# Kernel tuning notes

Hardware: AMD Instinct MI355X
Metric: run time of the kernel (lower is better)

The kernel has to match this reference:

```python
import jax, jax.numpy as jnp
import numpy as np

N_NODES = 100000
N_EDGES = 1000000
D_FEAT = 64
N_FILTER = 64
N_CLASSES = 16


def gcn_norm(edge_idx, n):
    """Add self-loops and compute symmetric normalization D^-1/2 (A+I) D^-1/2."""
    loop = jnp.arange(n, dtype=edge_idx.dtype)
    src = jnp.concatenate([edge_idx[0], loop])  # [E+N]
    dst = jnp.concatenate([edge_idx[1], loop])  # [E+N]
    w = jnp.ones(src.shape[0], dtype=jnp.float32)
    deg = jax.ops.segment_sum(w, dst, num_segments=n)  # in-degree incl. self-loop
    dinv = jnp.where(deg > 0, jax.lax.rsqrt(deg), 0.0)
    norm = dinv[src] * w * dinv[dst]  # [E+N]
    return src, dst, norm


def gcn_conv(x, W, b, src, dst, norm, n):
    h = x @ W                                   # [n, f] dense transform first (f <= d)
    msg = h[src] * norm[:, None]                # gather + scale  [E+N, f]
    out = jax.ops.segment_sum(msg, dst, num_segments=n)  # scatter-add  [n, f]
    return out + b


def setup_inputs() -> dict:
    key = jax.random.key(0)
    k1, k2, k3, k4 = jax.random.split(key, 4)
    X = jax.random.normal(k1, (N_NODES, D_FEAT), dtype=jnp.float32)
    edge_idx = jax.random.randint(k2, (2, N_EDGES), 0, N_NODES, dtype=jnp.int64)
    W1 = jax.random.normal(k3, (D_FEAT, N_FILTER), dtype=jnp.float32) * 0.05
    b1 = jnp.zeros((N_FILTER,), dtype=jnp.float32)
    W2 = jax.random.normal(k4, (N_FILTER, N_CLASSES), dtype=jnp.float32) * 0.05
    b2 = jnp.zeros((N_CLASSES,), dtype=jnp.float32)
    return {"X": X, "edge_idx": edge_idx, "W1": W1, "b1": b1, "W2": W2, "b2": b2}


def reference(X, edge_idx, W1, b1, W2, b2):
    n = X.shape[0]
    src, dst, norm = gcn_norm(edge_idx, n)
    x = gcn_conv(X, W1, b1, src, dst, norm, n)
    x = jax.nn.relu(x)
    # dropout p=0 -> identity
    x = gcn_conv(x, W2, b2, src, dst, norm, n)
    return x  # raw logits; pred_layer is not applied in the torch forward
```

## Files before the change

### kernel.cpp

```cpp
#include <hip/hip_runtime.h>
#include <hip/hip_bf16.h>


constexpr int N = 100000;
constexpr int E = 1000000;
constexpr int NB = (N + 511) / 512;
constexpr int CAP = 6144;
constexpr int CSTRIDE = 32;
constexpr int CHUNK = 2048;
constexpr int NBLK = (E + CHUNK - 1) / CHUNK;
constexpr int BT = 512;
constexpr int NPW = 6;
constexpr int NW = (N + NPW - 1) / NPW;
constexpr int NWBLK = (NW + 3) / 4;

__device__ __forceinline__ float bflo(unsigned u) { return __uint_as_float(u << 16); }
__device__ __forceinline__ float bfhi(unsigned u) { return __uint_as_float(u & 0xffff0000u); }

__device__ __forceinline__ void wait_lgkm0() {
    __builtin_amdgcn_s_waitcnt(0xc07f);
    __builtin_amdgcn_sched_barrier(0);
}

__global__ void k_bfill(const int* __restrict__ src, const int* __restrict__ dst,
                        int* __restrict__ cursor, int* __restrict__ bkt) {
    __shared__ int hist[256];
    __shared__ int lbase[256];
    __shared__ int gbase[256];
    __shared__ int lcur[256];
    __shared__ int ws[8];
    __shared__ int stage[CHUNK];
    __shared__ unsigned char sbkt[CHUNK];
    int t = threadIdx.x;
    int lane = t & 63;
    int e0 = blockIdx.x * CHUNK;
    int cnt = min(CHUNK, E - e0);

    if (t < 256) hist[t] = 0;
    __syncthreads();
    for (int j = t; j < cnt; j += BT)
        atomicAdd(&hist[dst[e0 + j] >> 9], 1);
    __syncthreads();
    int h = (t < 256) ? hist[t] : 0;
    int v = h;
#pragma unroll
    for (int off = 1; off < 64; off <<= 1) {
        int u = __shfl_up(v, off);
        if (lane >= off) v += u;
    }
    if (lane == 63) ws[t >> 6] = v;
    __syncthreads();
    int add = 0;
    for (int i = 0; i < (t >> 6); ++i) add += ws[i];
    int inc = v + add;
    if (t < 256) { lbase[t] = inc - h; lcur[t] = 0; }
    if (t < NB) gbase[t] = h ? atomicAdd(&cursor[t * CSTRIDE], h) : 0;
    __syncthreads();
    for (int j = t; j < cnt; j += BT) {
        int d = dst[e0 + j];
        int b = d >> 9;
        int pos = lbase[b] + atomicAdd(&lcur[b], 1);
        stage[pos] = ((d & 511) << 17) | src[e0 + j];
        sbkt[pos] = (unsigned char)b;
    }
    __syncthreads();
    for (int j = t; j < cnt; j += BT) {
        int b = sbkt[j];
        int gpos = gbase[b] + (j - lbase[b]);
        if (gpos < CAP) bkt[b * CAP + gpos] = stage[j];
    }
}

__global__ void k_bfine(const int* __restrict__ cursor, const int* __restrict__ bkt,
                        int* __restrict__ row_ptr, float* __restrict__ dinv,
                        int* __restrict__ csr_src) {
    __shared__ int cnt[512];
    __shared__ int excl[512];
    __shared__ int ws[8];
    int b = blockIdx.x;
    int t = threadIdx.x;
    int lane = t & 63;
    int c = (t < NB) ? cursor[t * CSTRIDE] : 0;
    int mv = (t < b) ? c : 0;
#pragma unroll
    for (int off = 1; off < 64; off <<= 1) mv += __shfl_xor(mv, off);
    if (lane == 0) ws[t >> 6] = mv;
    cnt[t] = 0;
    __syncthreads();
    int base = ws[0] + ws[1] + ws[2] + ws[3] + ws[4] + ws[5] + ws[6] + ws[7];
    int m = cursor[b * CSTRIDE];
    if (b == 0 && t == 0) row_ptr[N] = E;
    const int* bb = bkt + b * CAP;
    const int4* bb4 = (const int4*)bb;
    int m4 = m >> 2;
    for (int j = t; j < m4; j += BT) {
        int4 v = bb4[j];
        atomicAdd(&cnt[v.x >> 17], 1); atomicAdd(&cnt[v.y >> 17], 1);
        atomicAdd(&cnt[v.z >> 17], 1); atomicAdd(&cnt[v.w >> 17], 1);
    }
    for (int j = (m4 << 2) + t; j < m; j += BT) atomicAdd(&cnt[bb[j] >> 17], 1);
    __syncthreads();
    int h = cnt[t];
    int v = h;
#pragma unroll
    for (int off = 1; off < 64; off <<= 1) {
        int u = __shfl_up(v, off);
        if (lane >= off) v += u;
    }
    if (lane == 63) ws[t >> 6] = v;
    __syncthreads();
    int add = 0;
    for (int i = 0; i < (t >> 6); ++i) add += ws[i];
    int ex = v + add - h;
    excl[t] = ex;
    int node = b * 512 + t;
    if (node < N) {
        row_ptr[node] = base + ex;
        dinv[node] = rsqrtf((float)(h + 1));
    }
    __syncthreads();
    for (int j = t; j < m4; j += BT) {
        int4 v4 = bb4[j];
        int p0 = atomicAdd(&excl[v4.x >> 17], 1); csr_src[base + p0] = v4.x & 0x1FFFF;
        int p1 = atomicAdd(&excl[v4.y >> 17], 1); csr_src[base + p1] = v4.y & 0x1FFFF;
        int p2 = atomicAdd(&excl[v4.z >> 17], 1); csr_src[base + p2] = v4.z & 0x1FFFF;
        int p3 = atomicAdd(&excl[v4.w >> 17], 1); csr_src[base + p3] = v4.w & 0x1FFFF;
    }
    for (int j = (m4 << 2) + t; j < m; j += BT) {
        int vv = bb[j];
        int p = atomicAdd(&excl[vv >> 17], 1);
        csr_src[base + p] = vv & 0x1FFFF;
    }
}

__global__ void k_gemm1(const float* __restrict__ X, const float* __restrict__ W1,
                        const float* __restrict__ dinv, __hip_bfloat16* __restrict__ h1s,
                        __hip_bfloat16* __restrict__ h2s) {
    __shared__ float sX[4][4][64];
    int t = threadIdx.x;
    int lane = t & 63;
    int w = t >> 6;
    int wid = (blockIdx.x * 256 + t) >> 6;
    if (blockIdx.x == 0) {
        if (t < 64) h1s[(size_t)N * 64 + t] = __float2bfloat16(0.f);
        if (t < 16) h2s[(size_t)N * 16 + t] = __float2bfloat16(0.f);
    }
    float w1[64];
#pragma unroll
    for (int k = 0; k < 64; ++k) w1[k] = W1[k * 64 + lane];
    constexpr int STRIDE = 4096 * 4;
    int r4 = wid * 4;
    float x0 = X[(size_t)r4 * 64 + lane];
    float x1 = X[(size_t)(r4 + 1) * 64 + lane];
    float x2 = X[(size_t)(r4 + 2) * 64 + lane];
    float x3 = X[(size_t)(r4 + 3) * 64 + lane];
    for (; r4 < N; r4 += STRIDE) {
        int rn = r4 + STRIDE;
        float y0 = 0.f, y1 = 0.f, y2 = 0.f, y3 = 0.f;
        if (rn < N) {
            y0 = X[(size_t)rn * 64 + lane];
            y1 = X[(size_t)(rn + 1) * 64 + lane];
            y2 = X[(size_t)(rn + 2) * 64 + lane];
            y3 = X[(size_t)(rn + 3) * 64 + lane];
        }
        float dv0 = dinv[r4], dv1 = dinv[r4 + 1], dv2 = dinv[r4 + 2], dv3 = dinv[r4 + 3];
        sX[w][0][lane] = x0; sX[w][1][lane] = x1;
        sX[w][2][lane] = x2; sX[w][3][lane] = x3;
        wait_lgkm0();
        float acc0 = 0.f, acc1 = 0.f, acc2 = 0.f, acc3 = 0.f;
#pragma unroll
        for (int k = 0; k < 64; ++k) {
            float wk = w1[k];
            acc0 = fmaf(sX[w][0][k], wk, acc0);
            acc1 = fmaf(sX[w][1][k], wk, acc1);
            acc2 = fmaf(sX[w][2][k], wk, acc2);
            acc3 = fmaf(sX[w][3][k], wk, acc3);
        }
        acc0 *= dv0; acc1 *= dv1; acc2 *= dv2; acc3 *= dv3;
        float up0 = __shfl_xor(acc0, 1);
        float up1 = __shfl_xor(acc1, 1);
        float up2 = __shfl_xor(acc2, 1);
        float up3 = __shfl_xor(acc3, 1);
        if (!(lane & 1)) {
            __hip_bfloat162 p;
            p.x = __float2bfloat16(acc0); p.y = __float2bfloat16(up0);
            *(__hip_bfloat162*)(h1s + (size_t)r4 * 64 + lane) = p;
            p.x = __float2bfloat16(acc1); p.y = __float2bfloat16(up1);
            *(__hip_bfloat162*)(h1s + (size_t)(r4 + 1) * 64 + lane) = p;
            p.x = __float2bfloat16(acc2); p.y = __float2bfloat16(up2);
            *(__hip_bfloat162*)(h1s + (size_t)(r4 + 2) * 64 + lane) = p;
            p.x = __float2bfloat16(acc3); p.y = __float2bfloat16(up3);
            *(__hip_bfloat162*)(h1s + (size_t)(r4 + 3) * 64 + lane) = p;
        }
        x0 = y0; x1 = y1; x2 = y2; x3 = y3;
    }
}

__global__ void k_layer12(const int* __restrict__ row_ptr, const int* __restrict__ csr_src,
                          const float* __restrict__ dinv, const __hip_bfloat16* __restrict__ h1s,
                          const float* __restrict__ b1, const float* __restrict__ W2,
                          __hip_bfloat16* __restrict__ h2s) {
    __shared__ float sy[4][8][72];
    int t = threadIdx.x;
    int lane = t & 63;
    int w = t >> 6;
    int g8 = lane >> 3;
    int qo = (lane & 7) << 4;
    int g16 = lane >> 4, c16 = lane & 15;
    int wid = blockIdx.x * 4 + w;
    int d0 = wid * NPW;
    if (d0 >= N) return;
    int dend = min(d0 + NPW, N);
    float w2[16];
#pragma unroll
    for (int j = 0; j < 16; ++j) w2[j] = W2[(g16 * 16 + j) * 16 + c16];
    float b1v = b1[lane];
    const char* Hb = (const char*)h1s;

    int rp0 = row_ptr[d0];
    for (int d = d0; d < dend; ++d) {
        int rp1 = row_ptr[d + 1];
        float dv = dinv[d];
        float a[8] = {0, 0, 0, 0, 0, 0, 0, 0};
        if (g8 == 0) {
            uint4 u = *(const uint4*)(Hb + (((unsigned)d << 7) | qo));
            a[0] = bflo(u.x); a[1] = bfhi(u.x); a[2] = bflo(u.y); a[3] = bfhi(u.y);
            a[4] = bflo(u.z); a[5] = bfhi(u.z); a[6] = bflo(u.w); a[7] = bfhi(u.w);
        }
        for (int base = rp0; base < rp1; base += 64) {
            int nloc = min(64, rp1 - base);
            int sidx = (lane < nloc) ? csr_src[base + lane] : N;
            int steps = (nloc + 15) >> 4;
            for (int j = 0; j < steps; ++j) {
                int b0 = (j << 4) | g8;
                int s0 = __shfl(sidx, b0);
                int s1 = __shfl(sidx, b0 | 8);
                uint4 u0 = *(const uint4*)(Hb + (((unsigned)s0 << 7) | qo));
                uint4 u1 = *(const uint4*)(Hb + (((unsigned)s1 << 7) | qo));
                a[0] += bflo(u0.x); a[1] += bfhi(u0.x); a[2] += bflo(u0.y); a[3] += bfhi(u0.y);
                a[4] += bflo(u0.z); a[5] += bfhi(u0.z); a[6] += bflo(u0.w); a[7] += bfhi(u0.w);
                a[0] += bflo(u1.x); a[1] += bfhi(u1.x); a[2] += bflo(u1.y); a[3] += bfhi(u1.y);
                a[4] += bflo(u1.z); a[5] += bfhi(u1.z); a[6] += bflo(u1.w); a[7] += bfhi(u1.w);
            }
        }
        rp0 = rp1;
        float* row = &sy[w][g8][(lane & 7) << 3];
        *(float4*)row = make_float4(a[0], a[1], a[2], a[3]);
        *(float4*)(row + 4) = make_float4(a[4], a[5], a[6], a[7]);
        wait_lgkm0();
        float ysum = sy[w][0][lane] + sy[w][1][lane] + sy[w][2][lane] + sy[w][3][lane]
                   + sy[w][4][lane] + sy[w][5][lane] + sy[w][6][lane] + sy[w][7][lane];
        float y = fmaxf(fmaf(dv, ysum, b1v), 0.f);
        float o = 0.f;
#pragma unroll
        for (int j = 0; j < 16; ++j) o = fmaf(__shfl(y, (lane & 48) | j), w2[j], o);
        o += __shfl_xor(o, 16);
        o += __shfl_xor(o, 32);
        o *= dv;
        float oup = __shfl_xor(o, 1);
        if (lane < 16 && !(lane & 1)) {
            __hip_bfloat162 p;
            p.x = __float2bfloat16(o);
            p.y = __float2bfloat16(oup);
            *(__hip_bfloat162*)(h2s + (size_t)d * 16 + lane) = p;
        }
    }
}

__global__ void k_gather2(const int* __restrict__ row_ptr, const int* __restrict__ csr_src,
                          const float* __restrict__ dinv, const __hip_bfloat16* __restrict__ h2s,
                          const float* __restrict__ b2, float* __restrict__ out) {
    int t = threadIdx.x;
    int lane = t & 63;
    int g4 = lane >> 2;
    int q2 = lane & 3;
    int qo = q2 << 3;
    int wid = blockIdx.x * 4 + (t >> 6);
    int d0 = wid * NPW;
    if (d0 >= N) return;
    int dend = min(d0 + NPW, N);
    float b2v[4];
#pragma unroll
    for (int k = 0; k < 4; ++k) b2v[k] = b2[q2 * 4 + k];
    const char* Hb = (const char*)h2s;

    int rp0 = row_ptr[d0];
    for (int d = d0; d < dend; ++d) {
        int rp1 = row_ptr[d + 1];
        float dv = dinv[d];
        float a[4] = {0, 0, 0, 0};
        if (g4 == 0) {
            uint2 u = *(const uint2*)(Hb + (((unsigned)d << 5) | qo));
            a[0] = bflo(u.x); a[1] = bfhi(u.x); a[2] = bflo(u.y); a[3] = bfhi(u.y);
        }
        for (int base = rp0; base < rp1; base += 64) {
            int nloc = min(64, rp1 - base);
            int sidx = (lane < nloc) ? csr_src[base + lane] : N;
            int steps = (nloc + 15) >> 4;
            for (int j = 0; j < steps; ++j) {
                int s = __shfl(sidx, (j << 4) | g4);
                uint2 u = *(const uint2*)(Hb + (((unsigned)s << 5) | qo));
                a[0] += bflo(u.x); a[1] += bfhi(u.x);
                a[2] += bflo(u.y); a[3] += bfhi(u.y);
            }
        }
        rp0 = rp1;
#pragma unroll
        for (int k = 0; k < 4; ++k) {
            a[k] += __shfl_xor(a[k], 4);
            a[k] += __shfl_xor(a[k], 8);
            a[k] += __shfl_xor(a[k], 16);
            a[k] += __shfl_xor(a[k], 32);
        }
        if (lane < 4) {
            float4 r;
            r.x = fmaf(dv, a[0], b2v[0]);
            r.y = fmaf(dv, a[1], b2v[1]);
            r.z = fmaf(dv, a[2], b2v[2]);
            r.w = fmaf(dv, a[3], b2v[3]);
            *(float4*)(out + (size_t)d * 16 + q2 * 4) = r;
        }
    }
}

extern "C" void kernel_launch(void* const* d_in, const int* in_sizes, int n_in,
                              void* d_out, int out_size, void* d_ws, size_t ws_size,
                              hipStream_t stream) {
    const float* X  = (const float*)d_in[0];
    const int*   ei = (const int*)d_in[1];
    const float* W1 = (const float*)d_in[2];
    const float* b1 = (const float*)d_in[3];
    const float* W2 = (const float*)d_in[4];
    const float* b2 = (const float*)d_in[5];
    float* out = (float*)d_out;

    int* cursor  = (int*)d_ws;
    int* row_ptr = cursor + NB * CSTRIDE;
    int* bkt     = row_ptr + N + 4;
    int* csr_src = bkt + NB * CAP;
    float* dinv  = (float*)(csr_src + E);
    __hip_bfloat16* h1s = (__hip_bfloat16*)(dinv + N);
    __hip_bfloat16* h2s = h1s + (size_t)(N + 1) * 64;

    const int* src = ei;
    const int* dst = ei + E;

    hipMemsetAsync(cursor, 0, NB * CSTRIDE * sizeof(int), stream);
    k_bfill<<<NBLK, BT, 0, stream>>>(src, dst, cursor, bkt);
    k_bfine<<<NB, BT, 0, stream>>>(cursor, bkt, row_ptr, dinv, csr_src);
    k_gemm1<<<1024, 256, 0, stream>>>(X, W1, dinv, h1s, h2s);
    k_layer12<<<NWBLK, 256, 0, stream>>>(row_ptr, csr_src, dinv, h1s, b1, W2, h2s);
    k_gather2<<<NWBLK, 256, 0, stream>>>(row_ptr, csr_src, dinv, h2s, b2, out);
}
```

Before: 186.8 us.

## Batch per-warp edge index loads and prefetch next node's gathers in GCN layers

Both gather kernels now load row_ptr and dinv for all of a warp's nodes in one lane-parallel read. When the warp's total edge count fits in two 64-lane registers, they also load the whole csr_src range up front. The fast path software-pipelines the gathers: the first neighbour rows and self row for node k+1 are issued before node k's reduction and epilogue, hiding gather latency behind the serialized dependency chain. Warps with many edges fall back to the original loop. The cost is extra register pressure and more shuffles per neighbour select.

```diff
diff --git a/kernel.cpp b/kernel.cpp
--- a/kernel.cpp
+++ b/kernel.cpp
@@ -196,6 +196,11 @@
     }
 }
 
+__device__ __forceinline__ void acc8(float a[8], uint4 u) {
+    a[0] += bflo(u.x); a[1] += bfhi(u.x); a[2] += bflo(u.y); a[3] += bfhi(u.y);
+    a[4] += bflo(u.z); a[5] += bfhi(u.z); a[6] += bflo(u.w); a[7] += bfhi(u.w);
+}
+
 __global__ void k_layer12(const int* __restrict__ row_ptr, const int* __restrict__ csr_src,
                           const float* __restrict__ dinv, const __hip_bfloat16* __restrict__ h1s,
                           const float* __restrict__ b1, const float* __restrict__ W2,
@@ -210,17 +215,92 @@
     int wid = blockIdx.x * 4 + w;
     int d0 = wid * NPW;
     if (d0 >= N) return;
-    int dend = min(d0 + NPW, N);
+    int nd = min(NPW, N - d0);
     float w2[16];
 #pragma unroll
     for (int j = 0; j < 16; ++j) w2[j] = W2[(g16 * 16 + j) * 16 + c16];
     float b1v = b1[lane];
     const char* Hb = (const char*)h1s;
 
-    int rp0 = row_ptr[d0];
-    for (int d = d0; d < dend; ++d) {
-        int rp1 = row_ptr[d + 1];
-        float dv = dinv[d];
+    int rp_l = row_ptr[d0 + min(lane, nd)];
+    float dv_l = dinv[min(d0 + lane, N - 1)];
+    int rp_start = __shfl(rp_l, 0);
+    int nE = __shfl(rp_l, nd) - rp_start;
+
+    if (nE <= 112) {
+        int sidx0 = (lane < nE) ? csr_src[rp_start + lane] : N;
+        int sidx1 = (64 + lane < nE) ? csr_src[rp_start + 64 + lane] : N;
+        bool wide = nE > 64;
+        auto wsel = [&](int pos, int oend) -> int {
+            int s = __shfl(sidx0, pos & 63);
+            if (wide) {
+                int s1 = __shfl(sidx1, pos & 63);
+                if (pos >= 64) s = s1;
+            }
+            return (pos < oend) ? s : N;
+        };
+        int o0 = 0;
+        int o1 = __shfl(rp_l, 1) - rp_start;
+        int sA0 = wsel(o0 + g8, o1);
+        int sA1 = wsel(o0 + g8 + 8, o1);
+        uint4 uA0 = *(const uint4*)(Hb + (((unsigned)sA0 << 7) | qo));
+        uint4 uA1 = *(const uint4*)(Hb + (((unsigned)sA1 << 7) | qo));
+        uint4 uSA = {};
+        if (g8 == 0) uSA = *(const uint4*)(Hb + (((unsigned)d0 << 7) | qo));
+        for (int k = 0; k < nd; ++k) {
+            int d = d0 + k;
+            float dv = __shfl(dv_l, k);
+            int o0n = 0, o1n = 0;
+            uint4 uB0 = {}, uB1 = {}, uSB = {};
+            bool more = (k + 1 < nd);
+            if (more) {
+                o0n = __shfl(rp_l, k + 1) - rp_start;
+                o1n = __shfl(rp_l, k + 2) - rp_start;
+                int sB0 = wsel(o0n + g8, o1n);
+                int sB1 = wsel(o0n + g8 + 8, o1n);
+                uB0 = *(const uint4*)(Hb + (((unsigned)sB0 << 7) | qo));
+                uB1 = *(const uint4*)(Hb + (((unsigned)sB1 << 7) | qo));
+                if (g8 == 0) uSB = *(const uint4*)(Hb + (((unsigned)(d + 1) << 7) | qo));
+            }
+            float a[8] = {0, 0, 0, 0, 0, 0, 0, 0};
+            acc8(a, uA0); acc8(a, uA1);
+            if (g8 == 0) acc8(a, uSA);
+            for (int p = o0 + 16; p < o1; p += 16) {
+                int s0 = wsel(p + g8, o1);
+                int s1 = wsel(p + g8 + 8, o1);
+                uint4 u0 = *(const uint4*)(Hb + (((unsigned)s0 << 7) | qo));
+                uint4 u1 = *(const uint4*)(Hb + (((unsigned)s1 << 7) | qo));
+                acc8(a, u0); acc8(a, u1);
+            }
+            float* row = &sy[w][g8][(lane & 7) << 3];
+            *(float4*)row = make_float4(a[0], a[1], a[2], a[3]);
+            *(float4*)(row + 4) = make_float4(a[4], a[5], a[6], a[7]);
+            wait_lgkm0();
+            float ysum = sy[w][0][lane] + sy[w][1][lane] + sy[w][2][lane] + sy[w][3][lane]
+                       + sy[w][4][lane] + sy[w][5][lane] + sy[w][6][lane] + sy[w][7][lane];
+            float y = fmaxf(fmaf(dv, ysum, b1v), 0.f);
+            float o = 0.f;
+#pragma unroll
+            for (int j = 0; j < 16; ++j) o = fmaf(__shfl(y, (lane & 48) | j), w2[j], o);
+            o += __shfl_xor(o, 16);
+            o += __shfl_xor(o, 32);
+            o *= dv;
+            float oup = __shfl_xor(o, 1);
+            if (lane < 16 && !(lane & 1)) {
+                __hip_bfloat162 p;
+                p.x = __float2bfloat16(o);
+                p.y = __float2bfloat16(oup);
+                *(__hip_bfloat162*)(h2s + (size_t)d * 16 + lane) = p;
+            }
+            uA0 = uB0; uA1 = uB1; uSA = uSB; o0 = o0n; o1 = o1n;
+        }
+        return;
+    }
+    for (int k = 0; k < nd; ++k) {
+        int d = d0 + k;
+        int rp0 = __shfl(rp_l, k);
+        int rp1 = __shfl(rp_l, k + 1);
+        float dv = __shfl(dv_l, k);
         float a[8] = {0, 0, 0, 0, 0, 0, 0, 0};
         if (g8 == 0) {
             uint4 u = *(const uint4*)(Hb + (((unsigned)d << 7) | qo));
@@ -237,13 +317,9 @@
                 int s1 = __shfl(sidx, b0 | 8);
                 uint4 u0 = *(const uint4*)(Hb + (((unsigned)s0 << 7) | qo));
                 uint4 u1 = *(const uint4*)(Hb + (((unsigned)s1 << 7) | qo));
-                a[0] += bflo(u0.x); a[1] += bfhi(u0.x); a[2] += bflo(u0.y); a[3] += bfhi(u0.y);
-                a[4] += bflo(u0.z); a[5] += bfhi(u0.z); a[6] += bflo(u0.w); a[7] += bfhi(u0.w);
-                a[0] += bflo(u1.x); a[1] += bfhi(u1.x); a[2] += bflo(u1.y); a[3] += bfhi(u1.y);
-                a[4] += bflo(u1.z); a[5] += bfhi(u1.z); a[6] += bflo(u1.w); a[7] += bfhi(u1.w);
-            }
-        }
-        rp0 = rp1;
+                acc8(a, u0); acc8(a, u1);
+            }
+        }
         float* row = &sy[w][g8][(lane & 7) << 3];
         *(float4*)row = make_float4(a[0], a[1], a[2], a[3]);
         *(float4*)(row + 4) = make_float4(a[4], a[5], a[6], a[7]);
@@ -265,6 +341,10 @@
             *(__hip_bfloat162*)(h2s + (size_t)d * 16 + lane) = p;
         }
     }
+}
+
+__device__ __forceinline__ void acc4(float a[4], uint2 u) {
+    a[0] += bflo(u.x); a[1] += bfhi(u.x); a[2] += bflo(u.y); a[3] += bfhi(u.y);
 }
 
 __global__ void k_gather2(const int* __restrict__ row_ptr, const int* __restrict__ csr_src,
@@ -278,16 +358,80 @@
     int wid = blockIdx.x * 4 + (t >> 6);
     int d0 = wid * NPW;
     if (d0 >= N) return;
-    int dend = min(d0 + NPW, N);
+    int nd = min(NPW, N - d0);
     float b2v[4];
 #pragma unroll
     for (int k = 0; k < 4; ++k) b2v[k] = b2[q2 * 4 + k];
     const char* Hb = (const char*)h2s;
 
-    int rp0 = row_ptr[d0];
-    for (int d = d0; d < dend; ++d) {
-        int rp1 = row_ptr[d + 1];
-        float dv = dinv[d];
+    int rp_l = row_ptr[d0 + min(lane, nd)];
+    float dv_l = dinv[min(d0 + lane, N - 1)];
+    int rp_start = __shfl(rp_l, 0);
+    int nE = __shfl(rp_l, nd) - rp_start;
+
+    if (nE <= 112) {
+        int sidx0 = (lane < nE) ? csr_src[rp_start + lane] : N;
+        int sidx1 = (64 + lane < nE) ? csr_src[rp_start + 64 + lane] : N;
+        bool wide = nE > 64;
+        auto wsel = [&](int pos, int oend) -> int {
+            int s = __shfl(sidx0, pos & 63);
+            if (wide) {
+                int s1 = __shfl(sidx1, pos & 63);
+                if (pos >= 64) s = s1;
+            }
+            return (pos < oend) ? s : N;
+        };
+        int o0 = 0;
+        int o1 = __shfl(rp_l, 1) - rp_start;
+        int sA = wsel(o0 + g4, o1);
+        uint2 uA = *(const uint2*)(Hb + (((unsigned)sA << 5) | qo));
+        uint2 uSA = {};
+        if (g4 == 0) uSA = *(const uint2*)(Hb + (((unsigned)d0 << 5) | qo));
+        for (int k = 0; k < nd; ++k) {
+            int d = d0 + k;
+            float dv = __shfl(dv_l, k);
+            int o0n = 0, o1n = 0;
+            uint2 uB = {}, uSB = {};
+            bool more = (k + 1 < nd);
+            if (more) {
+                o0n = __shfl(rp_l, k + 1) - rp_start;
+                o1n = __shfl(rp_l, k + 2) - rp_start;
+                int sB = wsel(o0n + g4, o1n);
+                uB = *(const uint2*)(Hb + (((unsigned)sB << 5) | qo));
+                if (g4 == 0) uSB = *(const uint2*)(Hb + (((unsigned)(d + 1) << 5) | qo));
+            }
+            float a[4] = {0, 0, 0, 0};
+            acc4(a, uA);
+            if (g4 == 0) acc4(a, uSA);
+            for (int p = o0 + 16; p < o1; p += 16) {
+                int s = wsel(p + g4, o1);
+                uint2 u = *(const uint2*)(Hb + (((unsigned)s << 5) | qo));
+                acc4(a, u);
+            }
+#pragma unroll
+            for (int j = 0; j < 4; ++j) {
+                a[j] += __shfl_xor(a[j], 4);
+                a[j] += __shfl_xor(a[j], 8);
+                a[j] += __shfl_xor(a[j], 16);
+                a[j] += __shfl_xor(a[j], 32);
+            }
+            if (lane < 4) {
+                float4 r;
+                r.x = fmaf(dv, a[0], b2v[0]);
+                r.y = fmaf(dv, a[1], b2v[1]);
+                r.z = fmaf(dv, a[2], b2v[2]);
+                r.w = fmaf(dv, a[3], b2v[3]);
+                *(float4*)(out + (size_t)d * 16 + q2 * 4) = r;
+            }
+            uA = uB; uSA = uSB; o0 = o0n; o1 = o1n;
+        }
+        return;
+    }
+    for (int k = 0; k < nd; ++k) {
+        int d = d0 + k;
+        int rp0 = __shfl(rp_l, k);
+        int rp1 = __shfl(rp_l, k + 1);
+        float dv = __shfl(dv_l, k);
         float a[4] = {0, 0, 0, 0};
         if (g4 == 0) {
             uint2 u = *(const uint2*)(Hb + (((unsigned)d << 5) | qo));
@@ -300,17 +444,15 @@
             for (int j = 0; j < steps; ++j) {
                 int s = __shfl(sidx, (j << 4) | g4);
                 uint2 u = *(const uint2*)(Hb + (((unsigned)s << 5) | qo));
-                a[0] += bflo(u.x); a[1] += bfhi(u.x);
-                a[2] += bflo(u.y); a[3] += bfhi(u.y);
-            }
-        }
-        rp0 = rp1;
-#pragma unroll
-        for (int k = 0; k < 4; ++k) {
-            a[k] += __shfl_xor(a[k], 4);
-            a[k] += __shfl_xor(a[k], 8);
-            a[k] += __shfl_xor(a[k], 16);
-            a[k] += __shfl_xor(a[k], 32);
+                acc4(a, u);
+            }
+        }
+#pragma unroll
+        for (int j = 0; j < 4; ++j) {
+            a[j] += __shfl_xor(a[j], 4);
+            a[j] += __shfl_xor(a[j], 8);
+            a[j] += __shfl_xor(a[j], 16);
+            a[j] += __shfl_xor(a[j], 32);
         }
         if (lane < 4) {
             float4 r;
```

After: 188.5 us. About the same (+0.9%).

## Replace two-level bucket sort CSR build with global atomic histogram and scatter

Applied to the files above, without the earlier changes.

Replaces the bucketed two-pass counting sort (LDS staging into coarse buckets, then a per-bucket fine sort) with a plain CSR build. It runs a global per-node atomic histogram, a block-sum and scan, a row-pointer kernel that also seeds per-node cursors, and an atomic scatter of source ids. This drops the intermediate bucket buffer and its capacity limit, but adds more kernel launches and random global atomics on the destination counts and cursors. Edge order within each row becomes nondeterministic.

```diff
diff --git a/kernel.cpp b/kernel.cpp
--- a/kernel.cpp
+++ b/kernel.cpp
@@ -5,11 +5,6 @@
 constexpr int N = 100000;
 constexpr int E = 1000000;
 constexpr int NB = (N + 511) / 512;
-constexpr int CAP = 6144;
-constexpr int CSTRIDE = 32;
-constexpr int CHUNK = 2048;
-constexpr int NBLK = (E + CHUNK - 1) / CHUNK;
-constexpr int BT = 512;
 constexpr int NPW = 6;
 constexpr int NW = (N + NPW - 1) / NPW;
 constexpr int NWBLK = (NW + 3) / 4;
@@ -22,26 +17,33 @@
     __builtin_amdgcn_sched_barrier(0);
 }
 
-__global__ void k_bfill(const int* __restrict__ src, const int* __restrict__ dst,
-                        int* __restrict__ cursor, int* __restrict__ bkt) {
-    __shared__ int hist[256];
-    __shared__ int lbase[256];
-    __shared__ int gbase[256];
-    __shared__ int lcur[256];
+__global__ void k_hist(const int* __restrict__ dst, int* __restrict__ cnt) {
+    int i = blockIdx.x * blockDim.x + threadIdx.x;
+    int stride = gridDim.x * blockDim.x;
+    for (; i < E; i += stride) atomicAdd(&cnt[dst[i]], 1);
+}
+
+__global__ void k_bsum(const int* __restrict__ cnt, int* __restrict__ bsum) {
     __shared__ int ws[8];
-    __shared__ int stage[CHUNK];
-    __shared__ unsigned char sbkt[CHUNK];
-    int t = threadIdx.x;
-    int lane = t & 63;
-    int e0 = blockIdx.x * CHUNK;
-    int cnt = min(CHUNK, E - e0);
-
-    if (t < 256) hist[t] = 0;
+    int b = blockIdx.x, t = threadIdx.x, lane = t & 63;
+    int node = b * 512 + t;
+    int v = (node < N) ? cnt[node] : 0;
+#pragma unroll
+    for (int off = 1; off < 64; off <<= 1) v += __shfl_xor(v, off);
+    if (lane == 0) ws[t >> 6] = v;
     __syncthreads();
-    for (int j = t; j < cnt; j += BT)
-        atomicAdd(&hist[dst[e0 + j] >> 9], 1);
-    __syncthreads();
-    int h = (t < 256) ? hist[t] : 0;
+    if (t == 0) {
+        int s = 0;
+#pragma unroll
+        for (int i = 0; i < 8; ++i) s += ws[i];
+        bsum[b] = s;
+    }
+}
+
+__global__ void k_bscan(const int* __restrict__ bsum, int* __restrict__ bbase) {
+    __shared__ int ws[4];
+    int t = threadIdx.x, lane = t & 63;
+    int h = (t < NB) ? bsum[t] : 0;
     int v = h;
 #pragma unroll
     for (int off = 1; off < 64; off <<= 1) {
@@ -52,55 +54,16 @@
     __syncthreads();
     int add = 0;
     for (int i = 0; i < (t >> 6); ++i) add += ws[i];
-    int inc = v + add;
-    if (t < 256) { lbase[t] = inc - h; lcur[t] = 0; }
-    if (t < NB) gbase[t] = h ? atomicAdd(&cursor[t * CSTRIDE], h) : 0;
-    __syncthreads();
-    for (int j = t; j < cnt; j += BT) {
-        int d = dst[e0 + j];
-        int b = d >> 9;
-        int pos = lbase[b] + atomicAdd(&lcur[b], 1);
-        stage[pos] = ((d & 511) << 17) | src[e0 + j];
-        sbkt[pos] = (unsigned char)b;
-    }
-    __syncthreads();
-    for (int j = t; j < cnt; j += BT) {
-        int b = sbkt[j];
-        int gpos = gbase[b] + (j - lbase[b]);
-        if (gpos < CAP) bkt[b * CAP + gpos] = stage[j];
-    }
-}
-
-__global__ void k_bfine(const int* __restrict__ cursor, const int* __restrict__ bkt,
-                        int* __restrict__ row_ptr, float* __restrict__ dinv,
-                        int* __restrict__ csr_src) {
-    __shared__ int cnt[512];
-    __shared__ int excl[512];
+    if (t < NB) bbase[t] = v + add - h;
+}
+
+__global__ void k_rowptr(const int* __restrict__ cnt, const int* __restrict__ bbase,
+                         int* __restrict__ row_ptr, int* __restrict__ cursor,
+                         float* __restrict__ dinv) {
     __shared__ int ws[8];
-    int b = blockIdx.x;
-    int t = threadIdx.x;
-    int lane = t & 63;
-    int c = (t < NB) ? cursor[t * CSTRIDE] : 0;
-    int mv = (t < b) ? c : 0;
-#pragma unroll
-    for (int off = 1; off < 64; off <<= 1) mv += __shfl_xor(mv, off);
-    if (lane == 0) ws[t >> 6] = mv;
-    cnt[t] = 0;
-    __syncthreads();
-    int base = ws[0] + ws[1] + ws[2] + ws[3] + ws[4] + ws[5] + ws[6] + ws[7];
-    int m = cursor[b * CSTRIDE];
-    if (b == 0 && t == 0) row_ptr[N] = E;
-    const int* bb = bkt + b * CAP;
-    const int4* bb4 = (const int4*)bb;
-    int m4 = m >> 2;
-    for (int j = t; j < m4; j += BT) {
-        int4 v = bb4[j];
-        atomicAdd(&cnt[v.x >> 17], 1); atomicAdd(&cnt[v.y >> 17], 1);
-        atomicAdd(&cnt[v.z >> 17], 1); atomicAdd(&cnt[v.w >> 17], 1);
-    }
-    for (int j = (m4 << 2) + t; j < m; j += BT) atomicAdd(&cnt[bb[j] >> 17], 1);
-    __syncthreads();
-    int h = cnt[t];
+    int b = blockIdx.x, t = threadIdx.x, lane = t & 63;
+    int node = b * 512 + t;
+    int h = (node < N) ? cnt[node] : 0;
     int v = h;
 #pragma unroll
     for (int off = 1; off < 64; off <<= 1) {
@@ -112,24 +75,24 @@
     int add = 0;
     for (int i = 0; i < (t >> 6); ++i) add += ws[i];
     int ex = v + add - h;
-    excl[t] = ex;
-    int node = b * 512 + t;
     if (node < N) {
-        row_ptr[node] = base + ex;
+        int rp = bbase[b] + ex;
+        row_ptr[node] = rp;
+        cursor[node] = rp;
         dinv[node] = rsqrtf((float)(h + 1));
     }
-    __syncthreads();
-    for (int j = t; j < m4; j += BT) {
-        int4 v4 = bb4[j];
-        int p0 = atomicAdd(&excl[v4.x >> 17], 1); csr_src[base + p0] = v4.x & 0x1FFFF;
-        int p1 = atomicAdd(&excl[v4.y >> 17], 1); csr_src[base + p1] = v4.y & 0x1FFFF;
-        int p2 = atomicAdd(&excl[v4.z >> 17], 1); csr_src[base + p2] = v4.z & 0x1FFFF;
-        int p3 = atomicAdd(&excl[v4.w >> 17], 1); csr_src[base + p3] = v4.w & 0x1FFFF;
-    }
-    for (int j = (m4 << 2) + t; j < m; j += BT) {
-        int vv = bb[j];
-        int p = atomicAdd(&excl[vv >> 17], 1);
-        csr_src[base + p] = vv & 0x1FFFF;
+    if (b == 0 && t == 0) row_ptr[N] = E;
+}
+
+__global__ void k_scatter(const int* __restrict__ src, const int* __restrict__ dst,
+                          int* __restrict__ cursor, int* __restrict__ csr_src) {
+    int i = blockIdx.x * blockDim.x + threadIdx.x;
+    int stride = gridDim.x * blockDim.x;
+    for (; i < E; i += stride) {
+        int d = dst[i];
+        int s = src[i];
+        int pos = atomicAdd(&cursor[d], 1);
+        csr_src[pos] = s;
     }
 }
 
@@ -334,10 +297,12 @@
     const float* b2 = (const float*)d_in[5];
     float* out = (float*)d_out;
 
-    int* cursor  = (int*)d_ws;
-    int* row_ptr = cursor + NB * CSTRIDE;
-    int* bkt     = row_ptr + N + 4;
-    int* csr_src = bkt + NB * CAP;
+    int* cnt     = (int*)d_ws;
+    int* bsum    = cnt + N;
+    int* bbase   = bsum + 256;
+    int* row_ptr = bbase + 256;
+    int* cursor  = row_ptr + N + 4;
+    int* csr_src = cursor + N;
     float* dinv  = (float*)(csr_src + E);
     __hip_bfloat16* h1s = (__hip_bfloat16*)(dinv + N);
     __hip_bfloat16* h2s = h1s + (size_t)(N + 1) * 64;
@@ -345,9 +310,12 @@
     const int* src = ei;
     const int* dst = ei + E;
 
-    hipMemsetAsync(cursor, 0, NB * CSTRIDE * sizeof(int), stream);
-    k_bfill<<<NBLK, BT, 0, stream>>>(src, dst, cursor, bkt);
-    k_bfine<<<NB, BT, 0, stream>>>(cursor, bkt, row_ptr, dinv, csr_src);
+    hipMemsetAsync(cnt, 0, (N + 256) * sizeof(int), stream);
+    k_hist<<<1024, 512, 0, stream>>>(dst, cnt);
+    k_bsum<<<NB, 512, 0, stream>>>(cnt, bsum);
+    k_bscan<<<1, 256, 0, stream>>>(bsum, bbase);
+    k_rowptr<<<NB, 512, 0, stream>>>(cnt, bbase, row_ptr, cursor, dinv);
+    k_scatter<<<1024, 512, 0, stream>>>(src, dst, cursor, csr_src);
     k_gemm1<<<1024, 256, 0, stream>>>(X, W1, dinv, h1s, h2s);
     k_layer12<<<NWBLK, 256, 0, stream>>>(row_ptr, csr_src, dinv, h1s, b1, W2, h2s);
     k_gather2<<<NWBLK, 256, 0, stream>>>(row_ptr, csr_src, dinv, h2s, b2, out);
```

Measured after the change: 283.4 us. 1.52x slower.
